# Kernel optimization log

Measured on AMD Instinct MI355X. Metric: run time of the kernel, lower is better.

The kernel has to match this reference:

```python
import jax, jax.numpy as jnp
import numpy as np

HEADS = 8


def setup_inputs() -> dict:
    key = jax.random.key(0)
    k0, k1, k2, k3 = jax.random.split(key, 4)
    b, c, h, w = 8, 128, 32, 32
    x = jax.random.normal(k0, (b, c, h, w), dtype=jnp.float32)
    # torch nn.Linear weights: (out_features, in_features)
    s = c ** -0.5
    wq = jax.random.normal(k1, (c, c), dtype=jnp.float32) * s
    wk = jax.random.normal(k2, (c, c), dtype=jnp.float32) * s
    wv = jax.random.normal(k3, (c, c), dtype=jnp.float32) * s
    return {"x": x, "wq": wq, "wk": wk, "wv": wv}


def reference(x, wq, wk, wv):
    b, c, h, w = x.shape
    n = HEADS
    d = c // n
    scale = d ** -0.5
    xp = jnp.transpose(x, (0, 2, 3, 1))  # (b, h, w, c)
    # torch Linear: y = x @ W.T
    q = (xp @ wq.T).reshape(b, h, w, n, d)
    k = (xp @ wk.T).reshape(b, h, w, n, d)
    v = (xp @ wv.T).reshape(b, h, w, n, d)
    # full 2D spatial attention scores: (b, n, h, w, x, y)
    weights = jnp.einsum('bhwnd,bxynd->bnhwxy', q, k) * scale
    # NOTE: original softmaxes over the LAST spatial axis (y) only
    weights = jax.nn.softmax(weights, axis=-1)
    attn = jnp.einsum('bnhwxy,bxynd->bhwnd', weights, v)
    out = attn.reshape(b, h, w, c)
    return jnp.transpose(out, (0, 3, 1, 2))  # (b, c, h, w)
```

## Files before the change

### kernel.cpp

```cpp
#include <hip/hip_runtime.h>
#include <stdint.h>


typedef __bf16 bf16x8 __attribute__((ext_vector_type(8)));
typedef float f32x16 __attribute__((ext_vector_type(16)));

#define QOFF  0u
#define KOFF  (1u << 20)
#define VOFF  (2u << 20)

static __device__ __forceinline__ unsigned short f2bf(float f) {
  union { float f; uint32_t u; } v; v.f = f;
  uint32_t r = (v.u + 0x7FFFu + ((v.u >> 16) & 1u)) >> 16;
  return (unsigned short)r;
}
static __device__ __forceinline__ uint32_t pkrne(float lo, float hi) {
  return (uint32_t)f2bf(lo) | ((uint32_t)f2bf(hi) << 16);
}
static __device__ __forceinline__ uint32_t pktrunc(float lo, float hi) {
  return (__builtin_bit_cast(uint32_t, hi) & 0xffff0000u) |
         (__builtin_bit_cast(uint32_t, lo) >> 16);
}
static __device__ __forceinline__ float fexp2(float x) {
  float r;
  asm("v_exp_f32 %0, %1" : "=v"(r) : "v"(x));
  return r;
}
static __device__ __forceinline__ f32x16 zero16() {
  f32x16 z;
#pragma unroll
  for (int i = 0; i < 16; ++i) z[i] = 0.f;
  return z;
}
static __device__ __forceinline__ int perm23(int p) {
  return (p & ~12) | ((p & 4) << 1) | ((p & 8) >> 1);
}
static __device__ __forceinline__ bf16x8 pack8(float f0, float f1, float f2,
                                               float f3, float f4, float f5,
                                               float f6, float f7) {
  uint4 u = make_uint4(pkrne(f0, f1), pkrne(f2, f3), pkrne(f4, f5), pkrne(f6, f7));
  return __builtin_bit_cast(bf16x8, u);
}

__global__ __launch_bounds__(256) void proj_kernel(
    const float* __restrict__ x, const float* __restrict__ wq,
    const float* __restrict__ wk, const float* __restrict__ wv,
    unsigned short* __restrict__ ws) {
  int bid = blockIdx.x;
  int ptile = bid & 15;
  int mat = (bid >> 4) % 3;
  int b = bid / 48;
  int t = threadIdx.x;
  int wave = t >> 6, lane = t & 63;
  int h = lane >> 5, c = lane & 31;
  int out0 = wave * 32;

  const float* w = (mat == 0) ? wq : ((mat == 1) ? wk : wv);
  const float* wrow = w + (size_t)(out0 + c) * 128 + h * 8;
  const float* xcol = x + (size_t)b * 131072 + ptile * 64 + c;

  f32x16 acc0 = zero16(), acc1 = zero16();
#pragma unroll
  for (int kt = 0; kt < 8; ++kt) {
    int ch0 = kt * 16 + h * 8;
    float4 wa = *(const float4*)(wrow + kt * 16);
    float4 wb4 = *(const float4*)(wrow + kt * 16 + 4);
    float xb0[8], xb1[8];
#pragma unroll
    for (int j = 0; j < 8; ++j) {
      xb0[j] = xcol[(size_t)(ch0 + j) * 1024];
      xb1[j] = xcol[(size_t)(ch0 + j) * 1024 + 32];
    }
    bf16x8 af = pack8(wa.x, wa.y, wa.z, wa.w, wb4.x, wb4.y, wb4.z, wb4.w);
    bf16x8 b0 = pack8(xb0[0], xb0[1], xb0[2], xb0[3], xb0[4], xb0[5], xb0[6], xb0[7]);
    bf16x8 b1 = pack8(xb1[0], xb1[1], xb1[2], xb1[3], xb1[4], xb1[5], xb1[6], xb1[7]);
    acc0 = __builtin_amdgcn_mfma_f32_32x32x16_bf16(af, b0, acc0, 0, 0, 0);
    acc1 = __builtin_amdgcn_mfma_f32_32x32x16_bf16(af, b1, acc1, 0, 0, 0);
  }

  if (mat < 2) {
    float s = (mat == 0) ? 0.36067376022224085f : 1.0f;
    unsigned short* dst = ws + ((mat == 0) ? QOFF : KOFF);
#pragma unroll
    for (int nt = 0; nt < 2; ++nt) {
      f32x16 a = nt ? acc1 : acc0;
      int p = ptile * 64 + nt * 32 + c;
#pragma unroll
      for (int rg = 0; rg < 4; ++rg) {
        int bn = b * 8 + wave * 2 + (rg >> 1);
        int dbase = ((rg & 1) ? 8 : 0) + 4 * h;
        uint32_t lo = pkrne(a[rg * 4 + 0] * s, a[rg * 4 + 1] * s);
        uint32_t hi = pkrne(a[rg * 4 + 2] * s, a[rg * 4 + 3] * s);
        *(uint2*)(dst + (size_t)bn * 16384 + (size_t)p * 16 + dbase) =
            make_uint2(lo, hi);
      }
    }
  } else {
#pragma unroll
    for (int nt = 0; nt < 2; ++nt) {
      f32x16 a = nt ? acc1 : acc0;
      int p = ptile * 64 + nt * 32 + c;
      int pp = perm23(p);
#pragma unroll
      for (int r = 0; r < 16; ++r) {
        int moff = (r & 3) + 8 * (r >> 2) + 4 * h;
        int head = (out0 + moff) >> 4;
        int d = moff & 15;
        ws[VOFF + (size_t)(b * 8 + head) * 16384 + (size_t)d * 1024 + pp] =
            f2bf(a[r]);
      }
    }
  }
}

__global__ __launch_bounds__(256) void attn_kernel(
    const unsigned short* __restrict__ ws, float* __restrict__ out) {
  int bid = blockIdx.x;
  int qc = bid & 7, bn = bid >> 3;
  const unsigned short* Qg = ws + QOFF + (size_t)bn * 16384;
  const unsigned short* Kg = ws + KOFF + (size_t)bn * 16384;
  const unsigned short* Vg = ws + VOFF + (size_t)bn * 16384;

  int t = threadIdx.x;
  int wave = t >> 6, lane = t & 63;
  int h = lane >> 5, c = lane & 31;
  int q0 = qc * 128 + wave * 32;

  bf16x8 qb = __builtin_bit_cast(
      bf16x8, *(const uint4*)(Qg + (size_t)(q0 + c) * 16 + h * 8));

  const unsigned short* kbase = Kg + (size_t)c * 16 + h * 8;
  const unsigned short* vbase = Vg + (size_t)(c & 15) * 1024 + h * 8;

  f32x16 acc = zero16();
  uint4 kf  = *(const uint4*)(kbase);
  uint4 v0f = *(const uint4*)(vbase);
  uint4 v1f = *(const uint4*)(vbase + 16);

#pragma unroll 2
  for (int x = 0; x < 32; ++x) {
    bf16x8 ka  = __builtin_bit_cast(bf16x8, kf);
    bf16x8 va0 = __builtin_bit_cast(bf16x8, v0f);
    bf16x8 va1 = __builtin_bit_cast(bf16x8, v1f);
    if (x < 31) {
      kf  = *(const uint4*)(kbase + (x + 1) * 512);
      v0f = *(const uint4*)(vbase + (x + 1) * 32);
      v1f = *(const uint4*)(vbase + (x + 1) * 32 + 16);
    }

    f32x16 sv = __builtin_amdgcn_mfma_f32_32x32x16_bf16(ka, qb, zero16(), 0, 0, 0);

    float e[16];
#pragma unroll
    for (int r = 0; r < 16; ++r) e[r] = fexp2(sv[r]);
    float s0 = (e[0] + e[1]) + (e[2] + e[3]);
    float s1 = (e[4] + e[5]) + (e[6] + e[7]);
    float s2 = (e[8] + e[9]) + (e[10] + e[11]);
    float s3 = (e[12] + e[13]) + (e[14] + e[15]);
    float sum = (s0 + s1) + (s2 + s3);
    sum += __shfl_xor(sum, 32);
    float rs = __builtin_amdgcn_rcpf(sum);

    uint32_t pk[8];
#pragma unroll
    for (int j = 0; j < 8; ++j)
      pk[j] = pktrunc(e[2 * j] * rs, e[2 * j + 1] * rs);
    bf16x8 p0 = __builtin_bit_cast(bf16x8, make_uint4(pk[0], pk[1], pk[2], pk[3]));
    bf16x8 p1 = __builtin_bit_cast(bf16x8, make_uint4(pk[4], pk[5], pk[6], pk[7]));

    acc = __builtin_amdgcn_mfma_f32_32x32x16_bf16(va0, p0, acc, 0, 0, 0);
    acc = __builtin_amdgcn_mfma_f32_32x32x16_bf16(va1, p1, acc, 0, 0, 0);
  }

#pragma unroll
  for (int r = 0; r < 8; ++r) {
    int d = (r & 3) + 8 * (r >> 2) + 4 * h;
    out[(size_t)(bn * 16 + d) * 1024 + q0 + c] = acc[r];
  }
}

extern "C" void kernel_launch(void* const* d_in, const int* in_sizes, int n_in,
                              void* d_out, int out_size, void* d_ws, size_t ws_size,
                              hipStream_t stream) {
  const float* x  = (const float*)d_in[0];
  const float* wq = (const float*)d_in[1];
  const float* wk = (const float*)d_in[2];
  const float* wv = (const float*)d_in[3];
  unsigned short* ws = (unsigned short*)d_ws;
  float* out = (float*)d_out;

  proj_kernel<<<dim3(384), dim3(256), 0, stream>>>(x, wq, wk, wv, ws);
  attn_kernel<<<dim3(512), dim3(256), 0, stream>>>(ws, out);
}
```

Baseline: 96.42 us.

## Split attention x-loop across two blocks and combine with atomic adds

Splits the 32-step reduction over the key row axis x into two halves handled by separate blocks, doubling the attention grid to 1024 blocks. Partial results are combined with float atomicAdd into an output that a new zero kernel clears first. The PV accumulation also uses two independent accumulators to break the MFMA dependency chain. In exchange it adds an extra kernel launch, atomic traffic and re-reads of Q per block, and the summation order is no longer deterministic.

```diff
diff --git a/kernel.cpp b/kernel.cpp
--- a/kernel.cpp
+++ b/kernel.cpp
@@ -40,6 +40,10 @@
                                                float f6, float f7) {
   uint4 u = make_uint4(pkrne(f0, f1), pkrne(f2, f3), pkrne(f4, f5), pkrne(f6, f7));
   return __builtin_bit_cast(bf16x8, u);
+}
+
+__global__ __launch_bounds__(256) void zero_kernel(float4* __restrict__ out) {
+  out[(size_t)blockIdx.x * 256 + threadIdx.x] = make_float4(0.f, 0.f, 0.f, 0.f);
 }
 
 __global__ __launch_bounds__(256) void proj_kernel(
@@ -116,7 +120,9 @@
 __global__ __launch_bounds__(256) void attn_kernel(
     const unsigned short* __restrict__ ws, float* __restrict__ out) {
   int bid = blockIdx.x;
-  int qc = bid & 7, bn = bid >> 3;
+  int xh = bid & 1;
+  int qc = (bid >> 1) & 7;
+  int bn = bid >> 4;
   const unsigned short* Qg = ws + QOFF + (size_t)bn * 16384;
   const unsigned short* Kg = ws + KOFF + (size_t)bn * 16384;
   const unsigned short* Vg = ws + VOFF + (size_t)bn * 16384;
@@ -125,6 +131,7 @@
   int wave = t >> 6, lane = t & 63;
   int h = lane >> 5, c = lane & 31;
   int q0 = qc * 128 + wave * 32;
+  int x0 = xh * 16;
 
   bf16x8 qb = __builtin_bit_cast(
       bf16x8, *(const uint4*)(Qg + (size_t)(q0 + c) * 16 + h * 8));
@@ -132,18 +139,19 @@
   const unsigned short* kbase = Kg + (size_t)c * 16 + h * 8;
   const unsigned short* vbase = Vg + (size_t)(c & 15) * 1024 + h * 8;
 
-  f32x16 acc = zero16();
-  uint4 kf  = *(const uint4*)(kbase);
-  uint4 v0f = *(const uint4*)(vbase);
-  uint4 v1f = *(const uint4*)(vbase + 16);
+  f32x16 accA = zero16(), accB = zero16();
+  uint4 kf  = *(const uint4*)(kbase + (size_t)x0 * 512);
+  uint4 v0f = *(const uint4*)(vbase + x0 * 32);
+  uint4 v1f = *(const uint4*)(vbase + x0 * 32 + 16);
 
 #pragma unroll 2
-  for (int x = 0; x < 32; ++x) {
+  for (int xi = 0; xi < 16; ++xi) {
+    int x = x0 + xi;
     bf16x8 ka  = __builtin_bit_cast(bf16x8, kf);
     bf16x8 va0 = __builtin_bit_cast(bf16x8, v0f);
     bf16x8 va1 = __builtin_bit_cast(bf16x8, v1f);
-    if (x < 31) {
-      kf  = *(const uint4*)(kbase + (x + 1) * 512);
+    if (xi < 15) {
+      kf  = *(const uint4*)(kbase + (size_t)(x + 1) * 512);
       v0f = *(const uint4*)(vbase + (x + 1) * 32);
       v1f = *(const uint4*)(vbase + (x + 1) * 32 + 16);
     }
@@ -168,14 +176,14 @@
     bf16x8 p0 = __builtin_bit_cast(bf16x8, make_uint4(pk[0], pk[1], pk[2], pk[3]));
     bf16x8 p1 = __builtin_bit_cast(bf16x8, make_uint4(pk[4], pk[5], pk[6], pk[7]));
 
-    acc = __builtin_amdgcn_mfma_f32_32x32x16_bf16(va0, p0, acc, 0, 0, 0);
-    acc = __builtin_amdgcn_mfma_f32_32x32x16_bf16(va1, p1, acc, 0, 0, 0);
+    accA = __builtin_amdgcn_mfma_f32_32x32x16_bf16(va0, p0, accA, 0, 0, 0);
+    accB = __builtin_amdgcn_mfma_f32_32x32x16_bf16(va1, p1, accB, 0, 0, 0);
   }
 
 #pragma unroll
   for (int r = 0; r < 8; ++r) {
     int d = (r & 3) + 8 * (r >> 2) + 4 * h;
-    out[(size_t)(bn * 16 + d) * 1024 + q0 + c] = acc[r];
+    atomicAdd(out + (size_t)(bn * 16 + d) * 1024 + q0 + c, accA[r] + accB[r]);
   }
 }
 
@@ -189,6 +197,7 @@
   unsigned short* ws = (unsigned short*)d_ws;
   float* out = (float*)d_out;
 
+  zero_kernel<<<dim3(1024), dim3(256), 0, stream>>>((float4*)out);
   proj_kernel<<<dim3(384), dim3(256), 0, stream>>>(x, wq, wk, wv, ws);
-  attn_kernel<<<dim3(512), dim3(256), 0, stream>>>(ws, out);
-}
+  attn_kernel<<<dim3(1024), dim3(256), 0, stream>>>(ws, out);
+}
```

Result: no change. 95.32 us (-1.1%).
